# Kernel tuning notes

Hardware: AMD Instinct MI355X
Metric: run time of the kernel (lower is better)

## Reference

```python
import jax, jax.numpy as jnp
import numpy as np

B, S, D = 4, 4096, 256

def setup_inputs() -> dict:
    key = jax.random.key(0)
    ks = jax.random.split(key, 7)
    s = 1.0 / np.sqrt(D)
    return {
        "x": jax.random.normal(ks[0], (B, S, D), dtype=jnp.float32),
        "Wq": jax.random.normal(ks[1], (D, D), dtype=jnp.float32) * s,
        "bq": jax.random.normal(ks[2], (D,), dtype=jnp.float32) * s,
        "Wk": jax.random.normal(ks[3], (D, D), dtype=jnp.float32) * s,
        "bk": jax.random.normal(ks[4], (D,), dtype=jnp.float32) * s,
        "Wv": jax.random.normal(ks[5], (D, D), dtype=jnp.float32) * s,
        "bv": jax.random.normal(ks[6], (D,), dtype=jnp.float32) * s,
    }

def reference(x, Wq, bq, Wk, bk, Wv, bv):
    # nn.Linear: y = x @ W.T + b
    q = jnp.einsum('bsd,ed->bse', x, Wq) + bq  # [B,S,D]
    k = jnp.einsum('bsd,ed->bse', x, Wk) + bk  # [B,S,D]
    v = jnp.einsum('bsd,ed->bse', x, Wv) + bv  # [B,S,D]
    scale = 1.0 / jnp.sqrt(jnp.float32(x.shape[-1]))
    scores = jnp.einsum('bqd,bkd->bqk', q, k) * scale  # [B,S,S]
    attn = jax.nn.softmax(scores, axis=-1)
    return jnp.einsum('bqk,bkd->bqd', attn, v)
```

## Files before the change

kernel.cpp:

```cpp
#include <hip/hip_runtime.h>

typedef __attribute__((ext_vector_type(8))) short bf16x8;
typedef __attribute__((ext_vector_type(4))) short bf16x4;
typedef __attribute__((ext_vector_type(4))) float f32x4;
typedef __attribute__((ext_vector_type(16))) float f32x16;

#define MFMA16(a,b,c) __builtin_amdgcn_mfma_f32_16x16x32_bf16((a),(b),(c),0,0,0)
#define MFMA32(a,b,c) __builtin_amdgcn_mfma_f32_32x32x16_bf16((a),(b),(c),0,0,0)

__device__ __forceinline__ short f2bf(float f) {
  union { float f; unsigned u; } v; v.f = f;
  unsigned r = v.u + 0x7FFFu + ((v.u >> 16) & 1u);
  return (short)(r >> 16);
}
__device__ __forceinline__ float bf2f(short s) {
  union { unsigned u; float f; } v; v.u = ((unsigned)(unsigned short)s) << 16;
  return v.f;
}
__device__ __forceinline__ unsigned cvtpk(float lo, float hi) {
  unsigned d;
  asm("v_cvt_pk_bf16_f32 %0, %1, %2" : "=v"(d) : "v"(lo), "v"(hi));
  return d;
}
__device__ __forceinline__ void async16(const void* g, void* l) {
  __builtin_amdgcn_global_load_lds(
      (const __attribute__((address_space(1))) unsigned*)g,
      (__attribute__((address_space(3))) unsigned*)l, 16, 0, 0);
}

__global__ void cvt_w_kernel(const float* __restrict__ Wq, const float* __restrict__ Wk,
                             const float* __restrict__ Wv, short* __restrict__ Wb) {
  int v = blockIdx.x * 256 + threadIdx.x;
  int z = v >> 13, r = v & 8191;
  const float* src = ((z == 0) ? Wq : (z == 1) ? Wk : Wv) + r * 8;
  float4 a = *(const float4*)src;
  float4 b = *(const float4*)(src + 4);
  bf16x8 h;
  h[0]=f2bf(a.x); h[1]=f2bf(a.y); h[2]=f2bf(a.z); h[3]=f2bf(a.w);
  h[4]=f2bf(b.x); h[5]=f2bf(b.y); h[6]=f2bf(b.z); h[7]=f2bf(b.w);
  *(bf16x8*)(Wb + z * 65536 + r * 8) = h;
}

__global__ __launch_bounds__(256, 2) void proj_kernel(
    const float* __restrict__ x, const short* __restrict__ Wb,
    const float* __restrict__ bq, const float* __restrict__ bk, const float* __restrict__ bv,
    short* __restrict__ Qb, short* __restrict__ Kb, short* __restrict__ VTb)
{
  __shared__ __attribute__((aligned(16))) char xs[65536];
  const int tid = threadIdx.x;
  const int lane = tid & 63;
  const int w = tid >> 6;
  const int l15 = lane & 15, lg = lane >> 4;
  const int m0 = blockIdx.x * 128;
  const int batch = m0 >> 12;
  const int s0 = m0 & 4095;

  #pragma unroll
  for (int c = 0; c < 16; ++c) {
    int v = c * 256 + tid;
    int row = v >> 5, u = v & 31;
    const float* g = x + (size_t)(m0 + row) * 256 + u * 8;
    float4 a = *(const float4*)g;
    float4 b = *(const float4*)(g + 4);
    bf16x8 h;
    h[0]=f2bf(a.x); h[1]=f2bf(a.y); h[2]=f2bf(a.z); h[3]=f2bf(a.w);
    h[4]=f2bf(b.x); h[5]=f2bf(b.y); h[6]=f2bf(b.z); h[7]=f2bf(b.w);
    *(bf16x8*)(xs + row * 512 + ((u ^ (row & 7)) * 16)) = h;
  }
  __syncthreads();

  for (int z = 0; z < 3; ++z) {
    const short* Wz = Wb + z * 65536;
    bf16x8 wf[4][8];
    #pragma unroll
    for (int fc = 0; fc < 4; ++fc)
      #pragma unroll
      for (int ks = 0; ks < 8; ++ks)
        wf[fc][ks] = *(const bf16x8*)(Wz + (size_t)(w*64 + fc*16 + l15) * 256 + ks*32 + lg*8);

    if (z < 2) {
      const float* bias = z ? bk : bq;
      short* Ob = z ? Kb : Qb;
      const float scl = z ? 1.0f : 0.0625f;
      float bb[4];
      #pragma unroll
      for (int fc = 0; fc < 4; ++fc) bb[fc] = bias[w*64 + fc*16 + l15];
      #pragma unroll
      for (int ms = 0; ms < 8; ++ms) {
        bf16x8 xa[8];
        #pragma unroll
        for (int ks = 0; ks < 8; ++ks) {
          int row = ms * 16 + l15;
          xa[ks] = *(const bf16x8*)(xs + row * 512 + (((ks*4 + lg) ^ (row & 7)) * 16));
        }
        f32x4 acc[4];
        #pragma unroll
        for (int fc = 0; fc < 4; ++fc) acc[fc] = (f32x4){0.f,0.f,0.f,0.f};
        #pragma unroll
        for (int ks = 0; ks < 8; ++ks)
          #pragma unroll
          for (int fc = 0; fc < 4; ++fc)
            acc[fc] = MFMA16(xa[ks], wf[fc][ks], acc[fc]);
        #pragma unroll
        for (int fc = 0; fc < 4; ++fc)
          #pragma unroll
          for (int r = 0; r < 4; ++r)
            Ob[(size_t)(m0 + ms*16 + lg*4 + r) * 256 + w*64 + fc*16 + l15] =
                f2bf((acc[fc][r] + bb[fc]) * scl);
      }
    } else {
      float bvr[4][4];
      #pragma unroll
      for (int fr = 0; fr < 4; ++fr)
        #pragma unroll
        for (int r = 0; r < 4; ++r) bvr[fr][r] = bv[w*64 + fr*16 + lg*4 + r];
      #pragma unroll
      for (int ms = 0; ms < 8; ++ms) {
        bf16x8 xa[8];
        #pragma unroll
        for (int ks = 0; ks < 8; ++ks) {
          int row = ms * 16 + l15;
          xa[ks] = *(const bf16x8*)(xs + row * 512 + (((ks*4 + lg) ^ (row & 7)) * 16));
        }
        f32x4 acc[4];
        #pragma unroll
        for (int fr = 0; fr < 4; ++fr) acc[fr] = (f32x4){0.f,0.f,0.f,0.f};
        #pragma unroll
        for (int ks = 0; ks < 8; ++ks)
          #pragma unroll
          for (int fr = 0; fr < 4; ++fr)
            acc[fr] = MFMA16(wf[fr][ks], xa[ks], acc[fr]);
        #pragma unroll
        for (int fr = 0; fr < 4; ++fr)
          #pragma unroll
          for (int r = 0; r < 4; ++r) {
            int e = w*64 + fr*16 + lg*4 + r;
            VTb[(size_t)(batch*256 + e) * 4096 + s0 + ms*16 + l15] = f2bf(acc[fr][r] + bvr[fr][r]);
          }
      }
    }
  }
}

__global__ __launch_bounds__(512, 2) void attn_kernel(
    const short* __restrict__ Qb, const short* __restrict__ Kb,
    const short* __restrict__ VTb, short* __restrict__ Op, float* __restrict__ mlg)
{
  __shared__ __attribute__((aligned(16))) char smem[131072];
  const int tid = threadIdx.x;
  const int lane = tid & 63;
  const int w = tid >> 6;
  const int l31 = lane & 31, hi = lane >> 5;
  const int qs = w & 3, kh = w >> 2;

  const int b = blockIdx.x;
  const int xcd = b & 7;
  const int batch = xcd >> 1, ns = xcd & 1;
  const int qt = b >> 3;
  const int q0 = qt * 128;
  const int kvbase = ns * 2048;

  const char* Kg = (const char*)(Kb  + (size_t)batch * 4096 * 256);
  const char* Vg = (const char*)(VTb + (size_t)batch * 256 * 4096);

  bf16x8 qf[16];
  {
    const short* qrow = Qb + (size_t)(batch*4096 + q0 + qs*32 + l31) * 256;
    #pragma unroll
    for (int ks = 0; ks < 16; ++ks) qf[ks] = *(const bf16x8*)(qrow + ks*16 + hi*8);
  }

  f32x16 o[8];
  #pragma unroll
  for (int i = 0; i < 8; ++i)
    #pragma unroll
    for (int r = 0; r < 16; ++r) o[i][r] = 0.f;
  float m_run = -1e30f, l_run = 0.f;

  auto stage = [&](int buf, int kv0) {
    char* kl = smem + buf * 32768;
    #pragma unroll
    for (int c = 0; c < 4; ++c) {
      int v = c * 512 + tid;
      int row = v >> 5, s = v & 31;
      async16(Kg + (size_t)(kv0 + row) * 512 + ((s ^ (row & 7)) * 16),
              kl + (c * 512 + w * 64) * 16);
    }
    char* vl = smem + 65536 + buf * 32768;
    #pragma unroll
    for (int c = 0; c < 4; ++c) {
      int v = c * 512 + tid;
      int row = v >> 3, s = v & 7;
      async16(Vg + (size_t)row * 8192 + (size_t)kv0 * 2 + ((s ^ (row & 7)) * 16),
              vl + (c * 512 + w * 64) * 16);
    }
  };

  stage(0, kvbase);
  __syncthreads();

  for (int t = 0; t < 32; ++t) {
    const int cur = t & 1;
    if (t < 31) stage(cur ^ 1, kvbase + (t + 1) * 64);

    const char* kl = smem + cur * 32768;
    const char* vl = smem + 65536 + cur * 32768;

    f32x16 st;
    #pragma unroll
    for (int r = 0; r < 16; ++r) st[r] = 0.f;
    __builtin_amdgcn_s_setprio(1);
    #pragma unroll
    for (int ks = 0; ks < 16; ++ks) {
      int row = kh * 32 + l31;
      bf16x8 kf = *(const bf16x8*)(kl + row * 512 + (((ks*2 + hi) ^ (row & 7)) * 16));
      st = MFMA32(kf, qf[ks], st);
    }
    __builtin_amdgcn_s_setprio(0);

    float mx = st[0];
    #pragma unroll
    for (int r = 1; r < 16; ++r) mx = fmaxf(mx, st[r]);
    mx = fmaxf(mx, __shfl_xor(mx, 32));
    float m_new = fmaxf(m_run, mx);
    if (m_new > m_run) {
      float alpha = __expf(m_run - m_new);
      l_run *= alpha;
      #pragma unroll
      for (int df = 0; df < 8; ++df) o[df] = o[df] * alpha;
      m_run = m_new;
    }
    float lsum = 0.f;
    #pragma unroll
    for (int r = 0; r < 16; ++r) { st[r] = __expf(st[r] - m_run); lsum += st[r]; }
    l_run += lsum;

    bf16x8 pa[2];
    #pragma unroll
    for (int kvf = 0; kvf < 2; ++kvf) {
      float s0_ = st[8*kvf+0], s1_ = st[8*kvf+1], s2_ = st[8*kvf+2], s3_ = st[8*kvf+3];
      float s4_ = st[8*kvf+4], s5_ = st[8*kvf+5], s6_ = st[8*kvf+6], s7_ = st[8*kvf+7];
      unsigned X  = cvtpk(s0_, s1_);
      unsigned X2 = cvtpk(s2_, s3_);
      unsigned Y  = cvtpk(s4_, s5_);
      unsigned Y2 = cvtpk(s6_, s7_);
      unsigned Xs  = __shfl_xor((int)X, 32);
      unsigned X2s = __shfl_xor((int)X2, 32);
      unsigned Ys  = __shfl_xor((int)Y, 32);
      unsigned Y2s = __shfl_xor((int)Y2, 32);
      union { unsigned u[4]; bf16x8 v; } fr;
      fr.u[0] = hi ? Ys  : X;
      fr.u[1] = hi ? Y2s : X2;
      fr.u[2] = hi ? Y   : Xs;
      fr.u[3] = hi ? Y2  : X2s;
      pa[kvf] = fr.v;
    }

    __builtin_amdgcn_s_setprio(1);
    #pragma unroll
    for (int kvf = 0; kvf < 2; ++kvf) {
      #pragma unroll
      for (int df = 0; df < 8; ++df) {
        int row = df * 32 + l31;
        int u = (kh*2 + kvf) * 2 + hi;
        bf16x8 vb = *(const bf16x8*)(vl + row * 128 + ((u ^ (row & 7)) * 16));
        o[df] = MFMA32(vb, pa[kvf], o[df]);
      }
    }
    __builtin_amdgcn_s_setprio(0);

    __syncthreads();
  }

  float lt = l_run + __shfl_xor(l_run, 32);
  float* ml = (float*)smem;
  if (!hi) {
    float2 v = {m_run, lt};
    *(float2*)(ml + ((kh*4 + qs)*32 + l31)*2) = v;
  }
  __syncthreads();
  float2 other = *(const float2*)(ml + (((kh^1)*4 + qs)*32 + l31)*2);
  float m_star = fmaxf(m_run, other.x);
  float a_own = __expf(m_run - m_star);
  float l_star = a_own * lt + __expf(other.x - m_star) * other.y;
  char* xt = smem + 4096 + qs * 16384;

  if (kh == 1) {
    #pragma unroll
    for (int df = 0; df < 8; ++df)
      #pragma unroll
      for (int g = 0; g < 4; ++g) {
        bf16x4 pv;
        #pragma unroll
        for (int c = 0; c < 4; ++c) pv[c] = f2bf(o[df][4*g + c] * a_own);
        int u = (df*32 + 8*g + 4*hi) >> 2;
        *(bf16x4*)(xt + l31*512 + ((u ^ (l31 & 7)) * 8)) = pv;
      }
  }
  __syncthreads();
  if (kh == 0) {
    const int qglob = batch*4096 + q0 + qs*32 + l31;
    short* op = Op + ((size_t)ns * 16384 + qglob) * 256;
    #pragma unroll
    for (int df = 0; df < 8; ++df)
      #pragma unroll
      for (int g = 0; g < 4; ++g) {
        int u = (df*32 + 8*g + 4*hi) >> 2;
        bf16x4 p1 = *(const bf16x4*)(xt + l31*512 + ((u ^ (l31 & 7)) * 8));
        bf16x4 pv;
        #pragma unroll
        for (int c = 0; c < 4; ++c)
          pv[c] = f2bf(o[df][4*g + c] * a_own + bf2f(p1[c]));
        *(bf16x4*)(op + df*32 + 8*g + 4*hi) = pv;
      }
    if (!hi) {
      mlg[((size_t)ns*16384 + qglob)*2]     = m_star;
      mlg[((size_t)ns*16384 + qglob)*2 + 1] = l_star;
    }
  }
}

__global__ void combine_kernel(const short* __restrict__ Op, const float* __restrict__ mlg,
                               float* __restrict__ out) {
  int idx = blockIdx.x * 256 + threadIdx.x;
  int row = idx >> 5, c = idx & 31;
  float m0 = mlg[row * 2],           l0 = mlg[row * 2 + 1];
  float m1 = mlg[(16384 + row) * 2], l1 = mlg[(16384 + row) * 2 + 1];
  float ms = fmaxf(m0, m1);
  float a0 = __expf(m0 - ms), a1 = __expf(m1 - ms);
  float inv = 1.0f / (l0 * a0 + l1 * a1);
  a0 *= inv; a1 *= inv;
  bf16x8 v0 = *(const bf16x8*)(Op + (size_t)row * 256 + c * 8);
  bf16x8 v1 = *(const bf16x8*)(Op + (size_t)(16384 + row) * 256 + c * 8);
  float4 r0, r1;
  r0.x = a0*bf2f(v0[0]) + a1*bf2f(v1[0]);
  r0.y = a0*bf2f(v0[1]) + a1*bf2f(v1[1]);
  r0.z = a0*bf2f(v0[2]) + a1*bf2f(v1[2]);
  r0.w = a0*bf2f(v0[3]) + a1*bf2f(v1[3]);
  r1.x = a0*bf2f(v0[4]) + a1*bf2f(v1[4]);
  r1.y = a0*bf2f(v0[5]) + a1*bf2f(v1[5]);
  r1.z = a0*bf2f(v0[6]) + a1*bf2f(v1[6]);
  r1.w = a0*bf2f(v0[7]) + a1*bf2f(v1[7]);
  float* po = out + (size_t)row * 256 + c * 8;
  *(float4*)po = r0;
  *(float4*)(po + 4) = r1;
}

extern "C" void kernel_launch(void* const* d_in, const int* in_sizes, int n_in,
                              void* d_out, int out_size, void* d_ws, size_t ws_size,
                              hipStream_t stream) {
  const float* x  = (const float*)d_in[0];
  const float* Wq = (const float*)d_in[1];
  const float* bq = (const float*)d_in[2];
  const float* Wk = (const float*)d_in[3];
  const float* bk = (const float*)d_in[4];
  const float* Wv = (const float*)d_in[5];
  const float* bv = (const float*)d_in[6];
  float* out = (float*)d_out;

  char* ws = (char*)d_ws;
  short* Qb  = (short*)(ws);
  short* Kb  = (short*)(ws + 8388608);
  short* VTb = (short*)(ws + 16777216);
  short* Wb  = (short*)(ws + 25165824);
  float* mlg = (float*)(ws + 25559040);
  short* Op  = (short*)(ws + 25821184);

  cvt_w_kernel<<<dim3(96), dim3(256), 0, stream>>>(Wq, Wk, Wv, Wb);
  proj_kernel<<<dim3(128), dim3(256), 0, stream>>>(x, Wb, bq, bk, bv, Qb, Kb, VTb);
  attn_kernel<<<dim3(256), dim3(512), 0, stream>>>(Qb, Kb, VTb, Op, mlg);
  combine_kernel<<<dim3(2048), dim3(256), 0, stream>>>(Op, mlg, out);
}
```

Before: 214.4 us.

## Split projection per weight, 4-way KV split with 4-stage async pipeline

The projection kernel is split across Q/K/V into separate blocks with 64-row tiles (768 blocks instead of 128), and its output stores are vectorized. The attention kernel drops the intra-block KV halving. Each of its 8 waves now owns 32 query rows over a 1024-key quarter, using 32-key tiles in a 4-deep ring of async buffers with explicit vmcnt waits instead of double buffering plus syncthreads. The in-block merge of partial results is removed, and the combine kernel now merges four partial softmax results. This trades more partial output traffic and a heavier combine for better occupancy, less synchronization and deeper load latency hiding.

```diff
diff --git a/kernel.cpp b/kernel.cpp
--- a/kernel.cpp
+++ b/kernel.cpp
@@ -46,17 +46,19 @@
     const float* __restrict__ bq, const float* __restrict__ bk, const float* __restrict__ bv,
     short* __restrict__ Qb, short* __restrict__ Kb, short* __restrict__ VTb)
 {
-  __shared__ __attribute__((aligned(16))) char xs[65536];
+  __shared__ __attribute__((aligned(16))) char xs[32768];
   const int tid = threadIdx.x;
   const int lane = tid & 63;
   const int w = tid >> 6;
   const int l15 = lane & 15, lg = lane >> 4;
-  const int m0 = blockIdx.x * 128;
+  const int z = blockIdx.x >> 8;
+  const int mtile = blockIdx.x & 255;
+  const int m0 = mtile * 64;
   const int batch = m0 >> 12;
   const int s0 = m0 & 4095;
 
   #pragma unroll
-  for (int c = 0; c < 16; ++c) {
+  for (int c = 0; c < 8; ++c) {
     int v = c * 256 + tid;
     int row = v >> 5, u = v & 31;
     const float* g = x + (size_t)(m0 + row) * 256 + u * 8;
@@ -65,78 +67,77 @@
     bf16x8 h;
     h[0]=f2bf(a.x); h[1]=f2bf(a.y); h[2]=f2bf(a.z); h[3]=f2bf(a.w);
     h[4]=f2bf(b.x); h[5]=f2bf(b.y); h[6]=f2bf(b.z); h[7]=f2bf(b.w);
-    *(bf16x8*)(xs + row * 512 + ((u ^ (row & 7)) * 16)) = h;
+    *(bf16x8*)(xs + row * 512 + ((u ^ (row & 31)) * 16)) = h;
   }
   __syncthreads();
 
-  for (int z = 0; z < 3; ++z) {
-    const short* Wz = Wb + z * 65536;
-    bf16x8 wf[4][8];
+  const short* Wz = Wb + z * 65536;
+  bf16x8 wf[4][8];
+  #pragma unroll
+  for (int fc = 0; fc < 4; ++fc)
+    #pragma unroll
+    for (int ks = 0; ks < 8; ++ks)
+      wf[fc][ks] = *(const bf16x8*)(Wz + (size_t)(w*64 + fc*16 + l15) * 256 + ks*32 + lg*8);
+
+  if (z < 2) {
+    const float* bias = z ? bk : bq;
+    short* Ob = z ? Kb : Qb;
+    const float scl = z ? 1.0f : 0.0625f;
+    float bb[4][4];
     #pragma unroll
     for (int fc = 0; fc < 4; ++fc)
       #pragma unroll
+      for (int r = 0; r < 4; ++r) bb[fc][r] = bias[w*64 + fc*16 + lg*4 + r];
+    #pragma unroll
+    for (int ms = 0; ms < 4; ++ms) {
+      bf16x8 xa[8];
+      #pragma unroll
+      for (int ks = 0; ks < 8; ++ks) {
+        int row = ms * 16 + l15;
+        xa[ks] = *(const bf16x8*)(xs + row * 512 + (((ks*4 + lg) ^ (row & 31)) * 16));
+      }
+      f32x4 acc[4];
+      #pragma unroll
+      for (int fc = 0; fc < 4; ++fc) acc[fc] = (f32x4){0.f,0.f,0.f,0.f};
+      #pragma unroll
       for (int ks = 0; ks < 8; ++ks)
-        wf[fc][ks] = *(const bf16x8*)(Wz + (size_t)(w*64 + fc*16 + l15) * 256 + ks*32 + lg*8);
-
-    if (z < 2) {
-      const float* bias = z ? bk : bq;
-      short* Ob = z ? Kb : Qb;
-      const float scl = z ? 1.0f : 0.0625f;
-      float bb[4];
-      #pragma unroll
-      for (int fc = 0; fc < 4; ++fc) bb[fc] = bias[w*64 + fc*16 + l15];
-      #pragma unroll
-      for (int ms = 0; ms < 8; ++ms) {
-        bf16x8 xa[8];
-        #pragma unroll
-        for (int ks = 0; ks < 8; ++ks) {
-          int row = ms * 16 + l15;
-          xa[ks] = *(const bf16x8*)(xs + row * 512 + (((ks*4 + lg) ^ (row & 7)) * 16));
-        }
-        f32x4 acc[4];
-        #pragma unroll
-        for (int fc = 0; fc < 4; ++fc) acc[fc] = (f32x4){0.f,0.f,0.f,0.f};
-        #pragma unroll
-        for (int ks = 0; ks < 8; ++ks)
-          #pragma unroll
-          for (int fc = 0; fc < 4; ++fc)
-            acc[fc] = MFMA16(xa[ks], wf[fc][ks], acc[fc]);
         #pragma unroll
         for (int fc = 0; fc < 4; ++fc)
-          #pragma unroll
-          for (int r = 0; r < 4; ++r)
-            Ob[(size_t)(m0 + ms*16 + lg*4 + r) * 256 + w*64 + fc*16 + l15] =
-                f2bf((acc[fc][r] + bb[fc]) * scl);
-      }
-    } else {
-      float bvr[4][4];
-      #pragma unroll
-      for (int fr = 0; fr < 4; ++fr)
+          acc[fc] = MFMA16(wf[fc][ks], xa[ks], acc[fc]);
+      #pragma unroll
+      for (int fc = 0; fc < 4; ++fc) {
+        bf16x4 pv;
         #pragma unroll
-        for (int r = 0; r < 4; ++r) bvr[fr][r] = bv[w*64 + fr*16 + lg*4 + r];
-      #pragma unroll
-      for (int ms = 0; ms < 8; ++ms) {
-        bf16x8 xa[8];
+        for (int r = 0; r < 4; ++r) pv[r] = f2bf((acc[fc][r] + bb[fc][r]) * scl);
+        *(bf16x4*)(Ob + (size_t)(m0 + ms*16 + l15) * 256 + w*64 + fc*16 + lg*4) = pv;
+      }
+    }
+  } else {
+    float bvr[4];
+    #pragma unroll
+    for (int fc = 0; fc < 4; ++fc) bvr[fc] = bv[w*64 + fc*16 + l15];
+    #pragma unroll
+    for (int ms = 0; ms < 4; ++ms) {
+      bf16x8 xa[8];
+      #pragma unroll
+      for (int ks = 0; ks < 8; ++ks) {
+        int row = ms * 16 + l15;
+        xa[ks] = *(const bf16x8*)(xs + row * 512 + (((ks*4 + lg) ^ (row & 31)) * 16));
+      }
+      f32x4 acc[4];
+      #pragma unroll
+      for (int fc = 0; fc < 4; ++fc) acc[fc] = (f32x4){0.f,0.f,0.f,0.f};
+      #pragma unroll
+      for (int ks = 0; ks < 8; ++ks)
         #pragma unroll
-        for (int ks = 0; ks < 8; ++ks) {
-          int row = ms * 16 + l15;
-          xa[ks] = *(const bf16x8*)(xs + row * 512 + (((ks*4 + lg) ^ (row & 7)) * 16));
-        }
-        f32x4 acc[4];
+        for (int fc = 0; fc < 4; ++fc)
+          acc[fc] = MFMA16(xa[ks], wf[fc][ks], acc[fc]);
+      #pragma unroll
+      for (int fc = 0; fc < 4; ++fc) {
+        bf16x4 pv;
         #pragma unroll
-        for (int fr = 0; fr < 4; ++fr) acc[fr] = (f32x4){0.f,0.f,0.f,0.f};
-        #pragma unroll
-        for (int ks = 0; ks < 8; ++ks)
-          #pragma unroll
-          for (int fr = 0; fr < 4; ++fr)
-            acc[fr] = MFMA16(wf[fr][ks], xa[ks], acc[fr]);
-        #pragma unroll
-        for (int fr = 0; fr < 4; ++fr)
-          #pragma unroll
-          for (int r = 0; r < 4; ++r) {
-            int e = w*64 + fr*16 + lg*4 + r;
-            VTb[(size_t)(batch*256 + e) * 4096 + s0 + ms*16 + l15] = f2bf(acc[fr][r] + bvr[fr][r]);
-          }
+        for (int r = 0; r < 4; ++r) pv[r] = f2bf(acc[fc][r] + bvr[fc]);
+        *(bf16x4*)(VTb + (size_t)(batch*256 + w*64 + fc*16 + l15) * 4096 + s0 + ms*16 + lg*4) = pv;
       }
     }
   }
@@ -151,21 +152,20 @@
   const int lane = tid & 63;
   const int w = tid >> 6;
   const int l31 = lane & 31, hi = lane >> 5;
-  const int qs = w & 3, kh = w >> 2;
 
   const int b = blockIdx.x;
-  const int xcd = b & 7;
-  const int batch = xcd >> 1, ns = xcd & 1;
-  const int qt = b >> 3;
-  const int q0 = qt * 128;
-  const int kvbase = ns * 2048;
+  const int c = b & 15;
+  const int batch = c >> 2, ns = c & 3;
+  const int qt = b >> 4;
+  const int q0 = qt * 256;
+  const int kvbase = ns * 1024;
 
   const char* Kg = (const char*)(Kb  + (size_t)batch * 4096 * 256);
   const char* Vg = (const char*)(VTb + (size_t)batch * 256 * 4096);
 
   bf16x8 qf[16];
   {
-    const short* qrow = Qb + (size_t)(batch*4096 + q0 + qs*32 + l31) * 256;
+    const short* qrow = Qb + (size_t)(batch*4096 + q0 + w*32 + l31) * 256;
     #pragma unroll
     for (int ks = 0; ks < 16; ++ks) qf[ks] = *(const bf16x8*)(qrow + ks*16 + hi*8);
   }
@@ -180,31 +180,39 @@
   auto stage = [&](int buf, int kv0) {
     char* kl = smem + buf * 32768;
     #pragma unroll
-    for (int c = 0; c < 4; ++c) {
-      int v = c * 512 + tid;
+    for (int cc = 0; cc < 2; ++cc) {
+      int v = cc * 512 + tid;
       int row = v >> 5, s = v & 31;
-      async16(Kg + (size_t)(kv0 + row) * 512 + ((s ^ (row & 7)) * 16),
-              kl + (c * 512 + w * 64) * 16);
-    }
-    char* vl = smem + 65536 + buf * 32768;
-    #pragma unroll
-    for (int c = 0; c < 4; ++c) {
-      int v = c * 512 + tid;
-      int row = v >> 3, s = v & 7;
-      async16(Vg + (size_t)row * 8192 + (size_t)kv0 * 2 + ((s ^ (row & 7)) * 16),
-              vl + (c * 512 + w * 64) * 16);
+      async16(Kg + (size_t)(kvbase ? 0 : 0) + (size_t)(kv0 + row) * 512 + ((s ^ row) * 16),
+              kl + (size_t)v * 16);
+    }
+    char* vl = smem + buf * 32768 + 16384;
+    #pragma unroll
+    for (int cc = 0; cc < 2; ++cc) {
+      int v = cc * 512 + tid;
+      int sr = v >> 5, j = v & 31;
+      int jun = j ^ sr;
+      int d = sr * 8 + (jun >> 2), u = jun & 3;
+      async16(Vg + (size_t)d * 8192 + (size_t)kv0 * 2 + u * 16,
+              vl + (size_t)v * 16);
     }
   };
 
   stage(0, kvbase);
-  __syncthreads();
+  stage(1, kvbase + 32);
+  stage(2, kvbase + 64);
 
   for (int t = 0; t < 32; ++t) {
-    const int cur = t & 1;
-    if (t < 31) stage(cur ^ 1, kvbase + (t + 1) * 64);
-
-    const char* kl = smem + cur * 32768;
-    const char* vl = smem + 65536 + cur * 32768;
+    if (t < 30)       asm volatile("s_waitcnt vmcnt(8)" ::: "memory");
+    else if (t == 30) asm volatile("s_waitcnt vmcnt(4)" ::: "memory");
+    else              asm volatile("s_waitcnt vmcnt(0)" ::: "memory");
+    __builtin_amdgcn_sched_barrier(0);
+    __builtin_amdgcn_s_barrier();
+    __builtin_amdgcn_sched_barrier(0);
+    if (t < 29) stage((t + 3) & 3, kvbase + (t + 3) * 32);
+
+    const char* kl = smem + (t & 3) * 32768;
+    const char* vl = kl + 16384;
 
     f32x16 st;
     #pragma unroll
@@ -212,8 +220,7 @@
     __builtin_amdgcn_s_setprio(1);
     #pragma unroll
     for (int ks = 0; ks < 16; ++ks) {
-      int row = kh * 32 + l31;
-      bf16x8 kf = *(const bf16x8*)(kl + row * 512 + (((ks*2 + hi) ^ (row & 7)) * 16));
+      bf16x8 kf = *(const bf16x8*)(kl + l31 * 512 + (((ks*2 + hi) ^ l31) * 16));
       st = MFMA32(kf, qf[ks], st);
     }
     __builtin_amdgcn_s_setprio(0);
@@ -238,12 +245,10 @@
     bf16x8 pa[2];
     #pragma unroll
     for (int kvf = 0; kvf < 2; ++kvf) {
-      float s0_ = st[8*kvf+0], s1_ = st[8*kvf+1], s2_ = st[8*kvf+2], s3_ = st[8*kvf+3];
-      float s4_ = st[8*kvf+4], s5_ = st[8*kvf+5], s6_ = st[8*kvf+6], s7_ = st[8*kvf+7];
-      unsigned X  = cvtpk(s0_, s1_);
-      unsigned X2 = cvtpk(s2_, s3_);
-      unsigned Y  = cvtpk(s4_, s5_);
-      unsigned Y2 = cvtpk(s6_, s7_);
+      unsigned X  = cvtpk(st[8*kvf+0], st[8*kvf+1]);
+      unsigned X2 = cvtpk(st[8*kvf+2], st[8*kvf+3]);
+      unsigned Y  = cvtpk(st[8*kvf+4], st[8*kvf+5]);
+      unsigned Y2 = cvtpk(st[8*kvf+6], st[8*kvf+7]);
       unsigned Xs  = __shfl_xor((int)X, 32);
       unsigned X2s = __shfl_xor((int)X2, 32);
       unsigned Ys  = __shfl_xor((int)Y, 32);
@@ -261,62 +266,30 @@
     for (int kvf = 0; kvf < 2; ++kvf) {
       #pragma unroll
       for (int df = 0; df < 8; ++df) {
-        int row = df * 32 + l31;
-        int u = (kh*2 + kvf) * 2 + hi;
-        bf16x8 vb = *(const bf16x8*)(vl + row * 128 + ((u ^ (row & 7)) * 16));
+        int sr = df * 4 + (l31 >> 3);
+        int j = ((l31 & 7) * 4 + kvf * 2 + hi) ^ sr;
+        bf16x8 vb = *(const bf16x8*)(vl + sr * 512 + j * 16);
         o[df] = MFMA32(vb, pa[kvf], o[df]);
       }
     }
     __builtin_amdgcn_s_setprio(0);
-
-    __syncthreads();
   }
 
   float lt = l_run + __shfl_xor(l_run, 32);
-  float* ml = (float*)smem;
+  const int qglob = batch*4096 + q0 + w*32 + l31;
+  short* op = Op + ((size_t)ns * 16384 + qglob) * 256;
+  #pragma unroll
+  for (int df = 0; df < 8; ++df)
+    #pragma unroll
+    for (int g = 0; g < 4; ++g) {
+      bf16x4 pv;
+      #pragma unroll
+      for (int cc = 0; cc < 4; ++cc) pv[cc] = f2bf(o[df][4*g + cc]);
+      *(bf16x4*)(op + df*32 + 8*g + 4*hi) = pv;
+    }
   if (!hi) {
-    float2 v = {m_run, lt};
-    *(float2*)(ml + ((kh*4 + qs)*32 + l31)*2) = v;
-  }
-  __syncthreads();
-  float2 other = *(const float2*)(ml + (((kh^1)*4 + qs)*32 + l31)*2);
-  float m_star = fmaxf(m_run, other.x);
-  float a_own = __expf(m_run - m_star);
-  float l_star = a_own * lt + __expf(other.x - m_star) * other.y;
-  char* xt = smem + 4096 + qs * 16384;
-
-  if (kh == 1) {
-    #pragma unroll
-    for (int df = 0; df < 8; ++df)
-      #pragma unroll
-      for (int g = 0; g < 4; ++g) {
-        bf16x4 pv;
-        #pragma unroll
-        for (int c = 0; c < 4; ++c) pv[c] = f2bf(o[df][4*g + c] * a_own);
-        int u = (df*32 + 8*g + 4*hi) >> 2;
-        *(bf16x4*)(xt + l31*512 + ((u ^ (l31 & 7)) * 8)) = pv;
-      }
-  }
-  __syncthreads();
-  if (kh == 0) {
-    const int qglob = batch*4096 + q0 + qs*32 + l31;
-    short* op = Op + ((size_t)ns * 16384 + qglob) * 256;
-    #pragma unroll
-    for (int df = 0; df < 8; ++df)
-      #pragma unroll
-      for (int g = 0; g < 4; ++g) {
-        int u = (df*32 + 8*g + 4*hi) >> 2;
-        bf16x4 p1 = *(const bf16x4*)(xt + l31*512 + ((u ^ (l31 & 7)) * 8));
-        bf16x4 pv;
-        #pragma unroll
-        for (int c = 0; c < 4; ++c)
-          pv[c] = f2bf(o[df][4*g + c] * a_own + bf2f(p1[c]));
-        *(bf16x4*)(op + df*32 + 8*g + 4*hi) = pv;
-      }
-    if (!hi) {
-      mlg[((size_t)ns*16384 + qglob)*2]     = m_star;
-      mlg[((size_t)ns*16384 + qglob)*2 + 1] = l_star;
-    }
+    mlg[((size_t)ns*16384 + qglob)*2]     = m_run;
+    mlg[((size_t)ns*16384 + qglob)*2 + 1] = lt;
   }
 }
 
@@ -324,23 +297,28 @@
                                float* __restrict__ out) {
   int idx = blockIdx.x * 256 + threadIdx.x;
   int row = idx >> 5, c = idx & 31;
-  float m0 = mlg[row * 2],           l0 = mlg[row * 2 + 1];
-  float m1 = mlg[(16384 + row) * 2], l1 = mlg[(16384 + row) * 2 + 1];
-  float ms = fmaxf(m0, m1);
-  float a0 = __expf(m0 - ms), a1 = __expf(m1 - ms);
-  float inv = 1.0f / (l0 * a0 + l1 * a1);
-  a0 *= inv; a1 *= inv;
-  bf16x8 v0 = *(const bf16x8*)(Op + (size_t)row * 256 + c * 8);
-  bf16x8 v1 = *(const bf16x8*)(Op + (size_t)(16384 + row) * 256 + c * 8);
-  float4 r0, r1;
-  r0.x = a0*bf2f(v0[0]) + a1*bf2f(v1[0]);
-  r0.y = a0*bf2f(v0[1]) + a1*bf2f(v1[1]);
-  r0.z = a0*bf2f(v0[2]) + a1*bf2f(v1[2]);
-  r0.w = a0*bf2f(v0[3]) + a1*bf2f(v1[3]);
-  r1.x = a0*bf2f(v0[4]) + a1*bf2f(v1[4]);
-  r1.y = a0*bf2f(v0[5]) + a1*bf2f(v1[5]);
-  r1.z = a0*bf2f(v0[6]) + a1*bf2f(v1[6]);
-  r1.w = a0*bf2f(v0[7]) + a1*bf2f(v1[7]);
+  float m[4], l[4];
+  #pragma unroll
+  for (int p = 0; p < 4; ++p) {
+    m[p] = mlg[((size_t)p*16384 + row)*2];
+    l[p] = mlg[((size_t)p*16384 + row)*2 + 1];
+  }
+  float ms = fmaxf(fmaxf(m[0], m[1]), fmaxf(m[2], m[3]));
+  float a[4], den = 0.f;
+  #pragma unroll
+  for (int p = 0; p < 4; ++p) { a[p] = __expf(m[p] - ms); den += a[p]*l[p]; }
+  float inv = 1.0f / den;
+  float acc[8];
+  #pragma unroll
+  for (int j = 0; j < 8; ++j) acc[j] = 0.f;
+  #pragma unroll
+  for (int p = 0; p < 4; ++p) {
+    bf16x8 v = *(const bf16x8*)(Op + ((size_t)p*16384 + row)*256 + c*8);
+    #pragma unroll
+    for (int j = 0; j < 8; ++j) acc[j] += a[p] * bf2f(v[j]);
+  }
+  float4 r0 = {acc[0]*inv, acc[1]*inv, acc[2]*inv, acc[3]*inv};
+  float4 r1 = {acc[4]*inv, acc[5]*inv, acc[6]*inv, acc[7]*inv};
   float* po = out + (size_t)row * 256 + c * 8;
   *(float4*)po = r0;
   *(float4*)(po + 4) = r1;
@@ -364,10 +342,10 @@
   short* VTb = (short*)(ws + 16777216);
   short* Wb  = (short*)(ws + 25165824);
   float* mlg = (float*)(ws + 25559040);
-  short* Op  = (short*)(ws + 25821184);
+  short* Op  = (short*)(ws + 26083328);
 
   cvt_w_kernel<<<dim3(96), dim3(256), 0, stream>>>(Wq, Wk, Wv, Wb);
-  proj_kernel<<<dim3(128), dim3(256), 0, stream>>>(x, Wb, bq, bk, bv, Qb, Kb, VTb);
+  proj_kernel<<<dim3(768), dim3(256), 0, stream>>>(x, Wb, bq, bk, bv, Qb, Kb, VTb);
   attn_kernel<<<dim3(256), dim3(512), 0, stream>>>(Qb, Kb, VTb, Op, mlg);
   combine_kernel<<<dim3(2048), dim3(256), 0, stream>>>(Op, mlg, out);
 }
```

Result: slower. 225.5 us (+5.2%).
